# Kernel optimization log

Measured on AMD Instinct MI355X. Metric: run time of the kernel, lower is better.

The kernel has to match this reference:

```python
import jax, jax.numpy as jnp
import numpy as np

H = 128        # hidden_size
L = 3          # n_layers
VOCAB = 256    # input_size == output_size


def setup_inputs() -> dict:
    key = jax.random.key(0)
    ks = jax.random.split(key, 10)
    s = 1.0 / np.sqrt(H)  # PyTorch LSTM/Linear init scale
    return {
        "x": jax.random.randint(ks[0], (1,), 0, VOCAB),
        "h0": jax.random.normal(ks[1], (L, 1, H), dtype=jnp.float32),
        "c0": jax.random.normal(ks[2], (L, 1, H), dtype=jnp.float32),
        # params
        "emb": jax.random.normal(ks[3], (VOCAB, H), dtype=jnp.float32),
        "w_ih": jax.random.uniform(ks[4], (L, 4 * H, H), minval=-s, maxval=s, dtype=jnp.float32),
        "w_hh": jax.random.uniform(ks[5], (L, 4 * H, H), minval=-s, maxval=s, dtype=jnp.float32),
        "b_ih": jax.random.uniform(ks[6], (L, 4 * H), minval=-s, maxval=s, dtype=jnp.float32),
        "b_hh": jax.random.uniform(ks[7], (L, 4 * H), minval=-s, maxval=s, dtype=jnp.float32),
        "Wd": jax.random.uniform(ks[8], (VOCAB, H), minval=-s, maxval=s, dtype=jnp.float32),
        "bd": jax.random.uniform(ks[9], (VOCAB,), minval=-s, maxval=s, dtype=jnp.float32),
    }


def _lstm_step(inp, h0, c0, w_ih, w_hh, b_ih, b_hh):
    """Single time-step, 3-layer LSTM. inp: [1,H]; h0,c0: [L,1,H]. Dropout in eval mode (identity)."""
    hs, cs = [], []
    h_in = inp
    for l in range(L):
        # PyTorch gate order: input, forget, cell(g), output
        gates = h_in @ w_ih[l].T + h0[l] @ w_hh[l].T + b_ih[l] + b_hh[l]  # [1, 4H]
        i, f, g, o = jnp.split(gates, 4, axis=-1)
        c = jax.nn.sigmoid(f) * c0[l] + jax.nn.sigmoid(i) * jnp.tanh(g)
        h = jax.nn.sigmoid(o) * jnp.tanh(c)
        hs.append(h)
        cs.append(c)
        h_in = h  # inter-layer dropout (p=0.5) is identity in eval mode
    return h_in, jnp.stack(hs), jnp.stack(cs)


def reference(x, h0, c0, emb, w_ih, w_hh, b_ih, b_hh, Wd, bd):
    inp = emb[x].reshape(1, H)                      # encoder: [1, H]
    out, hn, cn = _lstm_step(inp, h0, c0, w_ih, w_hh, b_ih, b_hh)
    # self.dropout(p=0.1) identity in eval mode
    logits = out @ Wd.T + bd                        # decoder: [1, VOCAB]
    return logits, hn, cn
```

## Files before the change

### kernel.cpp

```cpp
#include <hip/hip_runtime.h>
#include <math.h>

#define H 128
#define NL 3
#define VOCAB 256
#define NBL 8
#define NLB (NL*NBL)
#define ND 2
#define NB_TOT (NLB+ND)

#define K_TAG(l) (0x51C0DE00u + (unsigned)(l))

typedef unsigned long long u64;

__device__ __forceinline__ float sigmoidf_(float x) {
    return 1.0f / (1.0f + __expf(-x));
}
__device__ __forceinline__ float fast_tanhf(float x) {
    const float e = __expf(2.0f * x);
    return 1.0f - 2.0f * __frcp_rn(e + 1.0f);
}

__global__ __launch_bounds__(256) void fused_lstm_kernel(
    const int*   __restrict__ x_idx,
    const float* __restrict__ h0,
    const float* __restrict__ c0,
    const float* __restrict__ emb,
    const float* __restrict__ w_ih,
    const float* __restrict__ w_hh,
    const float* __restrict__ b_ih,
    const float* __restrict__ b_hh,
    const float* __restrict__ Wd,
    const float* __restrict__ bd,
    float* __restrict__ logits,
    float* __restrict__ hn,
    float* __restrict__ cn,
    u64*   __restrict__ slots)
{
    __shared__ float s_in[H];
    __shared__ float s_h[H];
    __shared__ float s_gates[4][16];

    const int t   = threadIdx.x;
    const int bid = blockIdx.x;

    if (bid < NLB) {
        const int l  = bid >> 3;
        const int gb = bid & 7;
        const int row_local = t >> 2;
        const int chunk     = t & 3;
        const int g    = row_local >> 4;
        const int jr   = row_local & 15;
        const int unit = gb * 16 + jr;
        const int grow = g * H + unit;

        const size_t woff = ((size_t)l * 4 * H + grow) * H + chunk * 32;
        const float4* pi = (const float4*)(w_ih + woff);
        const float4* ph = (const float4*)(w_hh + woff);
        float4 wih[8], whh[8];
#pragma unroll
        for (int i = 0; i < 8; ++i) { wih[i] = pi[i]; whh[i] = ph[i]; }
        const float bias = b_ih[(size_t)l * 4 * H + grow]
                         + b_hh[(size_t)l * 4 * H + grow];
        float c0reg = 0.0f;
        if (t < 16) c0reg = c0[l * H + gb * 16 + t];
        if (t >= 128) s_h[t - 128] = h0[l * H + (t - 128)];
        if (l == 0 && t < H) s_in[t] = emb[(size_t)x_idx[0] * H + t];
        asm volatile("" ::: "memory");

        if (l > 0) {
            if (t < H) {
                const unsigned want = K_TAG(l - 1);
                u64 v;
                do {
                    v = __hip_atomic_load(&slots[(l - 1) * H + t],
                                          __ATOMIC_RELAXED,
                                          __HIP_MEMORY_SCOPE_AGENT);
                } while ((unsigned)(v >> 32) != want);
                s_in[t] = __uint_as_float((unsigned)v);
            }
        }
        __syncthreads();

        const float4* si = (const float4*)s_in;
        const float4* sh = (const float4*)s_h;
        float acc = 0.0f;
#pragma unroll
        for (int i = 0; i < 8; ++i) {
            float4 v = si[chunk * 8 + i], a = wih[i];
            acc = fmaf(a.x, v.x, acc);  acc = fmaf(a.y, v.y, acc);
            acc = fmaf(a.z, v.z, acc);  acc = fmaf(a.w, v.w, acc);
            float4 u = sh[chunk * 8 + i], b2 = whh[i];
            acc = fmaf(b2.x, u.x, acc); acc = fmaf(b2.y, u.y, acc);
            acc = fmaf(b2.z, u.z, acc); acc = fmaf(b2.w, u.w, acc);
        }
        acc += __shfl_xor(acc, 1);
        acc += __shfl_xor(acc, 2);
        if (chunk == 0) s_gates[g][jr] = acc + bias;
        __syncthreads();

        if (t < 16) {
            const int u = gb * 16 + t;
            const float iv = s_gates[0][t];
            const float fv = s_gates[1][t];
            const float gv = s_gates[2][t];
            const float ov = s_gates[3][t];
            const float c = sigmoidf_(fv) * c0reg + sigmoidf_(iv) * fast_tanhf(gv);
            const float h = sigmoidf_(ov) * fast_tanhf(c);
            cn[l * H + u] = c;
            hn[l * H + u] = h;
            const u64 w = ((u64)K_TAG(l) << 32) | (u64)__float_as_uint(h);
            __hip_atomic_store(&slots[l * H + u], w,
                               __ATOMIC_RELAXED, __HIP_MEMORY_SCOPE_AGENT);
        }
    } else {
        const int db        = bid - NLB;
        const int row_local = t >> 1;
        const int chunk     = t & 1;
        const int drow      = db * 128 + row_local;

        const float4* pw = (const float4*)(Wd + (size_t)drow * H + chunk * 64);
        float4 wd[16];
#pragma unroll
        for (int i = 0; i < 16; ++i) wd[i] = pw[i];
        const float bias = bd[drow];
        asm volatile("" ::: "memory");

        if (t < H) {
            const unsigned want = K_TAG(2);
            u64 v;
            do {
                v = __hip_atomic_load(&slots[2 * H + t],
                                      __ATOMIC_RELAXED,
                                      __HIP_MEMORY_SCOPE_AGENT);
            } while ((unsigned)(v >> 32) != want);
            s_h[t] = __uint_as_float((unsigned)v);
        }
        __syncthreads();

        const float4* sh = (const float4*)s_h;
        float acc = 0.0f;
#pragma unroll
        for (int i = 0; i < 16; ++i) {
            float4 v = sh[chunk * 16 + i], a = wd[i];
            acc = fmaf(a.x, v.x, acc); acc = fmaf(a.y, v.y, acc);
            acc = fmaf(a.z, v.z, acc); acc = fmaf(a.w, v.w, acc);
        }
        acc += __shfl_xor(acc, 1);
        if (chunk == 0) logits[drow] = acc + bias;
    }
}

extern "C" void kernel_launch(void* const* d_in, const int* in_sizes, int n_in,
                              void* d_out, int out_size, void* d_ws, size_t ws_size,
                              hipStream_t stream) {
    const int*   x    = (const int*)  d_in[0];
    const float* h0   = (const float*)d_in[1];
    const float* c0   = (const float*)d_in[2];
    const float* emb  = (const float*)d_in[3];
    const float* w_ih = (const float*)d_in[4];
    const float* w_hh = (const float*)d_in[5];
    const float* b_ih = (const float*)d_in[6];
    const float* b_hh = (const float*)d_in[7];
    const float* Wd   = (const float*)d_in[8];
    const float* bd   = (const float*)d_in[9];

    float* out    = (float*)d_out;
    float* logits = out;
    float* hn     = out + VOCAB;
    float* cn     = hn + NL * H;

    u64* slots = (u64*)d_ws;

    fused_lstm_kernel<<<NB_TOT, 256, 0, stream>>>(
        x, h0, c0, emb, w_ih, w_hh, b_ih, b_hh, Wd, bd,
        logits, hn, cn, slots);
}
```

Measured before the change: 10.03 us.

## Precompute recurrent h0 matvec before waiting on previous layer's output

The gate computation is split so the W_hh·h0 product plus biases is computed before the inter-layer spin-wait, by half the threads, while the other half wait on the previous layer's h and fill shared memory. After the wait, only the W_ih·input half remains on the critical path. The row split changes from four threads per row to two, so each computing thread holds more registers, and launch bounds now hint one block per unit. Only 128 threads per block compute, which halves arithmetic parallelism in exchange for shortening the dependency chain between layers.

```diff
diff --git a/kernel.cpp b/kernel.cpp
--- a/kernel.cpp
+++ b/kernel.cpp
@@ -21,7 +21,7 @@
     return 1.0f - 2.0f * __frcp_rn(e + 1.0f);
 }
 
-__global__ __launch_bounds__(256) void fused_lstm_kernel(
+__global__ __launch_bounds__(256, 1) void fused_lstm_kernel(
     const int*   __restrict__ x_idx,
     const float* __restrict__ h0,
     const float* __restrict__ c0,
@@ -38,7 +38,6 @@
     u64*   __restrict__ slots)
 {
     __shared__ float s_in[H];
-    __shared__ float s_h[H];
     __shared__ float s_gates[4][16];
 
     const int t   = threadIdx.x;
@@ -47,56 +46,73 @@
     if (bid < NLB) {
         const int l  = bid >> 3;
         const int gb = bid & 7;
-        const int row_local = t >> 2;
-        const int chunk     = t & 3;
-        const int g    = row_local >> 4;
-        const int jr   = row_local & 15;
-        const int unit = gb * 16 + jr;
-        const int grow = g * H + unit;
 
-        const size_t woff = ((size_t)l * 4 * H + grow) * H + chunk * 32;
-        const float4* pi = (const float4*)(w_ih + woff);
-        const float4* ph = (const float4*)(w_hh + woff);
-        float4 wih[8], whh[8];
+        float  r = 0.0f;
+        float4 wih[16];
+        float  c0reg = 0.0f;
+        int    half = 0, g = 0, jr = 0;
+
+        if (t < 128) {
+            const int row_local = t >> 1;
+            half = t & 1;
+            g    = row_local >> 4;
+            jr   = row_local & 15;
+            const int grow = g * H + gb * 16 + jr;
+            const size_t base = ((size_t)l * 4 * H + grow) * H + half * 64;
+
+            const float4* ph  = (const float4*)(w_hh + base);
+            const float4* pi  = (const float4*)(w_ih + base);
+            const float4* ph0 = (const float4*)(h0 + l * H + half * 64);
+
+            float4 whh[16], h0v[16];
 #pragma unroll
-        for (int i = 0; i < 8; ++i) { wih[i] = pi[i]; whh[i] = ph[i]; }
-        const float bias = b_ih[(size_t)l * 4 * H + grow]
-                         + b_hh[(size_t)l * 4 * H + grow];
-        float c0reg = 0.0f;
-        if (t < 16) c0reg = c0[l * H + gb * 16 + t];
-        if (t >= 128) s_h[t - 128] = h0[l * H + (t - 128)];
-        if (l == 0 && t < H) s_in[t] = emb[(size_t)x_idx[0] * H + t];
-        asm volatile("" ::: "memory");
+            for (int i = 0; i < 16; ++i) whh[i] = ph[i];
+#pragma unroll
+            for (int i = 0; i < 16; ++i) wih[i] = pi[i];
+#pragma unroll
+            for (int i = 0; i < 16; ++i) h0v[i] = ph0[i];
+            if (t < 16) c0reg = c0[l * H + gb * 16 + t];
 
-        if (l > 0) {
-            if (t < H) {
+            float acc = 0.0f;
+#pragma unroll
+            for (int i = 0; i < 16; ++i) {
+                float4 a = whh[i], v = h0v[i];
+                acc = fmaf(a.x, v.x, acc);  acc = fmaf(a.y, v.y, acc);
+                acc = fmaf(a.z, v.z, acc);  acc = fmaf(a.w, v.w, acc);
+            }
+            if (half == 0)
+                acc += b_ih[(size_t)l * 4 * H + grow]
+                     + b_hh[(size_t)l * 4 * H + grow];
+            r = acc;
+        } else {
+            const int tl = t - 128;
+            if (l == 0) {
+                s_in[tl] = emb[(size_t)x_idx[0] * H + tl];
+            } else {
                 const unsigned want = K_TAG(l - 1);
                 u64 v;
                 do {
-                    v = __hip_atomic_load(&slots[(l - 1) * H + t],
+                    v = __hip_atomic_load(&slots[(l - 1) * H + tl],
                                           __ATOMIC_RELAXED,
                                           __HIP_MEMORY_SCOPE_AGENT);
                 } while ((unsigned)(v >> 32) != want);
-                s_in[t] = __uint_as_float((unsigned)v);
+                s_in[tl] = __uint_as_float((unsigned)v);
             }
         }
         __syncthreads();
 
-        const float4* si = (const float4*)s_in;
-        const float4* sh = (const float4*)s_h;
-        float acc = 0.0f;
+        if (t < 128) {
+            const float4* si = (const float4*)s_in + half * 16;
+            float acc = r;
 #pragma unroll
-        for (int i = 0; i < 8; ++i) {
-            float4 v = si[chunk * 8 + i], a = wih[i];
-            acc = fmaf(a.x, v.x, acc);  acc = fmaf(a.y, v.y, acc);
-            acc = fmaf(a.z, v.z, acc);  acc = fmaf(a.w, v.w, acc);
-            float4 u = sh[chunk * 8 + i], b2 = whh[i];
-            acc = fmaf(b2.x, u.x, acc); acc = fmaf(b2.y, u.y, acc);
-            acc = fmaf(b2.z, u.z, acc); acc = fmaf(b2.w, u.w, acc);
+            for (int i = 0; i < 16; ++i) {
+                float4 a = wih[i], v = si[i];
+                acc = fmaf(a.x, v.x, acc);  acc = fmaf(a.y, v.y, acc);
+                acc = fmaf(a.z, v.z, acc);  acc = fmaf(a.w, v.w, acc);
+            }
+            acc += __shfl_xor(acc, 1);
+            if (half == 0) s_gates[g][jr] = acc;
         }
-        acc += __shfl_xor(acc, 1);
-        acc += __shfl_xor(acc, 2);
-        if (chunk == 0) s_gates[g][jr] = acc + bias;
         __syncthreads();
 
         if (t < 16) {
@@ -134,11 +150,11 @@
                                       __ATOMIC_RELAXED,
                                       __HIP_MEMORY_SCOPE_AGENT);
             } while ((unsigned)(v >> 32) != want);
-            s_h[t] = __uint_as_float((unsigned)v);
+            s_in[t] = __uint_as_float((unsigned)v);
         }
         __syncthreads();
 
-        const float4* sh = (const float4*)s_h;
+        const float4* sh = (const float4*)s_in;
         float acc = 0.0f;
 #pragma unroll
         for (int i = 0; i < 16; ++i) {
```

After: 9.664 us. -3.7%, faster.

## Precompute recurrent h0 dot before waiting on previous layer; gather gates via shuffles

Applied to the files above, without the earlier changes.

Each layer block now computes the W_hh·h0 partial sum before spinning on the previous layer's output. Only the W_ih·input half stays on the critical dependency chain. The thread mapping is changed so all four gates of a unit sit in one wavefront. Gate values are gathered with __shfl instead of a shared-memory round trip and a second __syncthreads, and the pointwise work is spread across lanes in every wavefront. The extra __syncthreads before the spin loop adds a barrier but allows the independent work to overlap the wait.

```diff
diff --git a/kernel.cpp b/kernel.cpp
--- a/kernel.cpp
+++ b/kernel.cpp
@@ -39,7 +39,6 @@
 {
     __shared__ float s_in[H];
     __shared__ float s_h[H];
-    __shared__ float s_gates[4][16];
 
     const int t   = threadIdx.x;
     const int bid = blockIdx.x;
@@ -47,26 +46,40 @@
     if (bid < NLB) {
         const int l  = bid >> 3;
         const int gb = bid & 7;
-        const int row_local = t >> 2;
-        const int chunk     = t & 3;
-        const int g    = row_local >> 4;
-        const int jr   = row_local & 15;
-        const int unit = gb * 16 + jr;
-        const int grow = g * H + unit;
 
-        const size_t woff = ((size_t)l * 4 * H + grow) * H + chunk * 32;
-        const float4* pi = (const float4*)(w_ih + woff);
-        const float4* ph = (const float4*)(w_hh + woff);
+        const int ul    = t >> 4;
+        const int g     = (t >> 2) & 3;
+        const int chunk = t & 3;
+        const int unit  = gb * 16 + ul;
+        const int grow  = g * H + unit;
+
+        const size_t base = ((size_t)l * 4 * H + grow) * H + chunk * 32;
+        const float4* pi = (const float4*)(w_ih + base);
+        const float4* ph = (const float4*)(w_hh + base);
         float4 wih[8], whh[8];
 #pragma unroll
         for (int i = 0; i < 8; ++i) { wih[i] = pi[i]; whh[i] = ph[i]; }
-        const float bias = b_ih[(size_t)l * 4 * H + grow]
-                         + b_hh[(size_t)l * 4 * H + grow];
+        float bias = 0.0f;
+        if (chunk == 0) bias = b_ih[(size_t)l * 4 * H + grow]
+                             + b_hh[(size_t)l * 4 * H + grow];
         float c0reg = 0.0f;
-        if (t < 16) c0reg = c0[l * H + gb * 16 + t];
-        if (t >= 128) s_h[t - 128] = h0[l * H + (t - 128)];
-        if (l == 0 && t < H) s_in[t] = emb[(size_t)x_idx[0] * H + t];
-        asm volatile("" ::: "memory");
+        if ((t & 15) == 0) c0reg = c0[l * H + unit];
+
+        if (t >= 128) {
+            const int tl = t - 128;
+            s_h[tl] = h0[l * H + tl];
+            if (l == 0) s_in[tl] = emb[(size_t)x_idx[0] * H + tl];
+        }
+        __syncthreads();
+
+        const float4* sh = (const float4*)s_h + chunk * 8;
+        float r = bias;
+#pragma unroll
+        for (int i = 0; i < 8; ++i) {
+            float4 a = whh[i], v = sh[i];
+            r = fmaf(a.x, v.x, r);  r = fmaf(a.y, v.y, r);
+            r = fmaf(a.z, v.z, r);  r = fmaf(a.w, v.w, r);
+        }
 
         if (l > 0) {
             if (t < H) {
@@ -82,35 +95,28 @@
         }
         __syncthreads();
 
-        const float4* si = (const float4*)s_in;
-        const float4* sh = (const float4*)s_h;
-        float acc = 0.0f;
+        const float4* si = (const float4*)s_in + chunk * 8;
+        float acc = r;
 #pragma unroll
         for (int i = 0; i < 8; ++i) {
-            float4 v = si[chunk * 8 + i], a = wih[i];
+            float4 a = wih[i], v = si[i];
             acc = fmaf(a.x, v.x, acc);  acc = fmaf(a.y, v.y, acc);
             acc = fmaf(a.z, v.z, acc);  acc = fmaf(a.w, v.w, acc);
-            float4 u = sh[chunk * 8 + i], b2 = whh[i];
-            acc = fmaf(b2.x, u.x, acc); acc = fmaf(b2.y, u.y, acc);
-            acc = fmaf(b2.z, u.z, acc); acc = fmaf(b2.w, u.w, acc);
         }
         acc += __shfl_xor(acc, 1);
         acc += __shfl_xor(acc, 2);
-        if (chunk == 0) s_gates[g][jr] = acc + bias;
-        __syncthreads();
-
-        if (t < 16) {
-            const int u = gb * 16 + t;
-            const float iv = s_gates[0][t];
-            const float fv = s_gates[1][t];
-            const float gv = s_gates[2][t];
-            const float ov = s_gates[3][t];
+        const int bl = (t & 63) & 48;
+        const float iv = __shfl(acc, bl,      64);
+        const float fv = __shfl(acc, bl + 4,  64);
+        const float gv = __shfl(acc, bl + 8,  64);
+        const float ov = __shfl(acc, bl + 12, 64);
+        if ((t & 15) == 0) {
             const float c = sigmoidf_(fv) * c0reg + sigmoidf_(iv) * fast_tanhf(gv);
             const float h = sigmoidf_(ov) * fast_tanhf(c);
-            cn[l * H + u] = c;
-            hn[l * H + u] = h;
+            cn[l * H + unit] = c;
+            hn[l * H + unit] = h;
             const u64 w = ((u64)K_TAG(l) << 32) | (u64)__float_as_uint(h);
-            __hip_atomic_store(&slots[l * H + u], w,
+            __hip_atomic_store(&slots[l * H + unit], w,
                                __ATOMIC_RELAXED, __HIP_MEMORY_SCOPE_AGENT);
         }
     } else {
@@ -134,15 +140,15 @@
                                       __ATOMIC_RELAXED,
                                       __HIP_MEMORY_SCOPE_AGENT);
             } while ((unsigned)(v >> 32) != want);
-            s_h[t] = __uint_as_float((unsigned)v);
+            s_in[t] = __uint_as_float((unsigned)v);
         }
         __syncthreads();
 
-        const float4* sh = (const float4*)s_h;
+        const float4* sh = (const float4*)s_in + chunk * 16;
         float acc = 0.0f;
 #pragma unroll
         for (int i = 0; i < 16; ++i) {
-            float4 v = sh[chunk * 16 + i], a = wd[i];
+            float4 a = wd[i], v = sh[i];
             acc = fmaf(a.x, v.x, acc); acc = fmaf(a.y, v.y, acc);
             acc = fmaf(a.z, v.z, acc); acc = fmaf(a.w, v.w, acc);
         }
```

New measurement: 10.82 us. +7.9%, slower.
